# Optimization experiments

Hardware: AMD Instinct MI355X
Metric: run time of the kernel (lower is better)

## Reference

```python
import jax, jax.numpy as jnp
import numpy as np

DEPTH = 4  # truncation depth of the signature


def setup_inputs() -> dict:
    key = jax.random.key(0)
    # (N, L, C) batch of paths
    path = jax.random.normal(key, (32, 256, 8), dtype=jnp.float32)
    return {"path": path}


def _signature(path, depth):
    """Truncated path signature via Chen's relation over linear segments.

    For a linear segment with increment dx, its signature is exp(dx) in the
    tensor algebra: level j = dx^{\otimes j} / j!.  The signature of the
    concatenated path is the tensor-algebra product of segment signatures,
    computed with a scan over segments.
    """
    N, L, C = path.shape
    dx = path[:, 1:, :] - path[:, :-1, :]  # (N, L-1, C) increments

    def exp_levels(d):
        # levels of exp(d): e_j = d^{\otimes j} / j!, flattened to (N, C^j)
        levels = [d]
        for j in range(2, depth + 1):
            nxt = jnp.einsum('na,nb->nab', levels[-1], d).reshape(N, -1) / j
            levels.append(nxt)
        return levels

    def step(carry, d):
        # carry: tuple of (N, C^k) for k = 1..depth (levels of running signature)
        # Chen: new_k = sum_{i+j=k} carry_i (x) e_j, with carry_0 = e_0 = 1
        e = exp_levels(d)
        new = []
        for k in range(1, depth + 1):
            acc = carry[k - 1] + e[k - 1]  # i=k,j=0 and i=0,j=k terms
            for i in range(1, k):
                acc = acc + jnp.einsum(
                    'na,nb->nab', carry[i - 1], e[k - i - 1]
                ).reshape(N, -1)
            new.append(acc)
        return tuple(new), None

    init = tuple(jnp.zeros((N, C ** k), path.dtype) for k in range(1, depth + 1))
    final, _ = jax.lax.scan(step, init, jnp.swapaxes(dx, 0, 1))  # scan over L-1
    return jnp.concatenate(final, axis=-1)  # (N, C + C^2 + ... + C^depth)


def reference(path):
    return _signature(path, DEPTH)
```

## Files before the change

### kernel.cpp

```cpp
#include <hip/hip_runtime.h>

#define NBATCH 32
#define LPATH 256
#define NSEG 255
#define SIGLEN 4680
#define INV6 (1.0f/6.0f)
#define INV24 (1.0f/24.0f)

typedef float v2f __attribute__((ext_vector_type(2)));

struct __align__(16) CBuf {
    float T4t2[64 * 64];
    float T3b[8 * 68];
    float T2[64];
    float T1[8];
};

__device__ __forceinline__ void publish_sig(CBuf& B, const v2f S4v[32],
                                            const float S3[8], float S2, float a1a,
                                            int l, int a, int b) {
    #pragma unroll
    for (int ch = 0; ch < 32; ++ch)
        *(v2f*)&B.T4t2[ch * 128 + 2 * l] = S4v[ch];
    #pragma unroll
    for (int c = 0; c < 8; ++c)
        B.T3b[a * 68 + b * 8 + c] = S3[c];
    B.T2[l] = S2;
    if (b == 0) B.T1[a] = a1a;
}

__device__ __forceinline__ void absorb_sig(const CBuf& B, v2f S4v[32], float S3[8],
                                           float& S2, float& a1a, int l, int a, int b) {
    v2f t1v[4];
    #pragma unroll
    for (int h = 0; h < 4; ++h) t1v[h] = *(const v2f*)&B.T1[2 * h];
    const float t1a = B.T1[a];
    const float t1b = B.T1[b];
    const v2f S2v = S2, a1v = a1a;
    #pragma unroll
    for (int c = 0; c < 8; ++c) {
        const v2f S3cv = S3[c];
        #pragma unroll
        for (int h = 0; h < 4; ++h) {
            const v2f t2v = *(const v2f*)&B.T2[c * 8 + 2 * h];
            const v2f t3v = *(const v2f*)&B.T3b[b * 68 + c * 8 + 2 * h];
            const v2f t4v = *(const v2f*)&B.T4t2[(c * 4 + h) * 128 + 2 * l];
            v2f acc = S4v[c * 4 + h] + t4v;
            acc = __builtin_elementwise_fma(S3cv, t1v[h], acc);
            acc = __builtin_elementwise_fma(S2v, t2v, acc);
            acc = __builtin_elementwise_fma(a1v, t3v, acc);
            S4v[c * 4 + h] = acc;
        }
    }
    #pragma unroll
    for (int c = 0; c < 8; ++c)
        S3[c] += S2 * B.T1[c] + a1a * B.T2[b * 8 + c] + B.T3b[a * 68 + b * 8 + c];
    S2 += a1a * t1b + B.T2[l];
    a1a += t1a;
}

__global__ __launch_bounds__(512, 2) void sig_kernel(const float* __restrict__ path,
                                                     float* __restrict__ out) {
    const int n = blockIdx.x;
    const int t = threadIdx.x;
    const int w = t >> 6, l = t & 63, a = l >> 3, b = l & 7;

    __shared__ CBuf bufs[4];
    __shared__ float dbuf[2048];

    const float* prow = path + n * (LPATH * 8);
    {
        const int i4 = t * 4;
        if (i4 < NSEG * 8) {
            const float4 x0 = *(const float4*)&prow[i4];
            const float4 x1 = *(const float4*)&prow[i4 + 8];
            *(float4*)&dbuf[i4] = make_float4(x1.x - x0.x, x1.y - x0.y,
                                              x1.z - x0.z, x1.w - x0.w);
        } else {
            *(float4*)&dbuf[i4] = make_float4(0.f, 0.f, 0.f, 0.f);
        }
    }
    __syncthreads();

    v2f S4v[32];
    float S3[8];
    #pragma unroll
    for (int j = 0; j < 32; ++j) S4v[j] = (v2f)0.f;
    #pragma unroll
    for (int c = 0; c < 8; ++c) S3[c] = 0.f;
    float S2 = 0.f, a1a = 0.f;

    const float* wbase = &dbuf[w << 8];
    const float* abase = wbase + a;
    const float* bbase = wbase + b;

    #pragma unroll
    for (int ss = 0; ss < 32; ++ss) {
        const float4 dlo = *(const float4*)&wbase[ss * 8];
        const float4 dhi = *(const float4*)&wbase[ss * 8 + 4];
        const v2f dp[4] = {{dlo.x, dlo.y}, {dlo.z, dlo.w},
                           {dhi.x, dhi.y}, {dhi.z, dhi.w}};
        const float da = abase[ss * 8];
        const float db = bbase[ss * 8];
        const float dab = da * db;
        const float P = dab * INV24 + a1a * db * INV6 + S2 * 0.5f;
        const float Q = dab * INV6  + a1a * db * 0.5f + S2;
        const v2f Pv = P, Qv = Q;
        v2f Kv[4];
        #pragma unroll
        for (int h = 0; h < 4; ++h) {
            v2f S3h = {S3[2 * h], S3[2 * h + 1]};
            Kv[h] = __builtin_elementwise_fma(dp[h], Pv, S3h);
            S3h = __builtin_elementwise_fma(dp[h], Qv, S3h);
            S3[2 * h] = S3h.x; S3[2 * h + 1] = S3h.y;
        }
        #pragma unroll
        for (int c = 0; c < 8; ++c) {
            const float Kc = (c & 1) ? Kv[c >> 1].y : Kv[c >> 1].x;
            const v2f Kcv = Kc;
            #pragma unroll
            for (int h = 0; h < 4; ++h)
                S4v[c * 4 + h] = __builtin_elementwise_fma(dp[h], Kcv, S4v[c * 4 + h]);
        }
        S2 += db * (da * 0.5f + a1a);
        a1a += da;
    }

    #pragma unroll
    for (int r = 0; r < 3; ++r) {
        const int stride = 1 << r;
        const int m = (stride << 1) - 1;
        if ((w & m) == stride)
            publish_sig(bufs[w >> (r + 1)], S4v, S3, S2, a1a, l, a, b);
        __syncthreads();
        if ((w & m) == 0)
            absorb_sig(bufs[w >> (r + 1)], S4v, S3, S2, a1a, l, a, b);
        __syncthreads();
    }

    if (w == 0) {
        float* o = out + n * SIGLEN;
        if (b == 0) o[a] = a1a;
        o[8 + l] = S2;
        *(float4*)&o[72 + l * 8]     = make_float4(S3[0], S3[1], S3[2], S3[3]);
        *(float4*)&o[72 + l * 8 + 4] = make_float4(S3[4], S3[5], S3[6], S3[7]);
        #pragma unroll
        for (int ch = 0; ch < 32; ++ch)
            *(v2f*)&o[584 + l * 64 + 2 * ch] = S4v[ch];
    }
}

extern "C" void kernel_launch(void* const* d_in, const int* in_sizes, int n_in,
                              void* d_out, int out_size, void* d_ws, size_t ws_size,
                              hipStream_t stream) {
    const float* path = (const float*)d_in[0];
    float* out = (float*)d_out;
    sig_kernel<<<NBATCH, 512, 0, stream>>>(path, out);
}
```

Measured before the change: 17.95 us.

## Split each path over two blocks with half-channel waves and cross-block combine

```diff
diff --git a/kernel.cpp b/kernel.cpp
--- a/kernel.cpp
+++ b/kernel.cpp
@@ -4,149 +4,237 @@
 #define LPATH 256
 #define NSEG 255
 #define SIGLEN 4680
+#define PIMG 4712
+#define PSTRF 4720
 #define INV6 (1.0f/6.0f)
 #define INV24 (1.0f/24.0f)
 
 typedef float v2f __attribute__((ext_vector_type(2)));
+typedef unsigned long long u64;
+typedef unsigned int u32;
 
 struct __align__(16) CBuf {
-    float T4t2[64 * 64];
-    float T3b[8 * 68];
+    float T4t2[4096];
+    float T3b[544];
     float T2[64];
     float T1[8];
 };
 
-__device__ __forceinline__ void publish_sig(CBuf& B, const v2f S4v[32],
-                                            const float S3[8], float S2, float a1a,
-                                            int l, int a, int b) {
-    #pragma unroll
-    for (int ch = 0; ch < 32; ++ch)
-        *(v2f*)&B.T4t2[ch * 128 + 2 * l] = S4v[ch];
-    #pragma unroll
-    for (int c = 0; c < 8; ++c)
-        B.T3b[a * 68 + b * 8 + c] = S3[c];
-    B.T2[l] = S2;
-    if (b == 0) B.T1[a] = a1a;
-}
-
-__device__ __forceinline__ void absorb_sig(const CBuf& B, v2f S4v[32], float S3[8],
-                                           float& S2, float& a1a, int l, int a, int b) {
+__device__ __forceinline__ void publish_half(CBuf& B, const v2f S4v[16],
+                                             const float S3[4], float S2, float a1a,
+                                             int l, int a, int b, int h) {
+    #pragma unroll
+    for (int ci = 0; ci < 4; ++ci)
+        #pragma unroll
+        for (int eh = 0; eh < 4; ++eh)
+            *(v2f*)&B.T4t2[((4*h + ci)*4 + eh)*128 + 2*l] = S4v[ci*4 + eh];
+    #pragma unroll
+    for (int ci = 0; ci < 4; ++ci)
+        B.T3b[a*68 + b*8 + 4*h + ci] = S3[ci];
+    if (h == 0) {
+        B.T2[l] = S2;
+        if (b == 0) B.T1[a] = a1a;
+    }
+}
+
+__device__ __forceinline__ void absorb_half(const CBuf& B, v2f S4v[16], float S3[4],
+                                            float& S2, float& a1a,
+                                            int l, int a, int b, int h) {
     v2f t1v[4];
     #pragma unroll
-    for (int h = 0; h < 4; ++h) t1v[h] = *(const v2f*)&B.T1[2 * h];
-    const float t1a = B.T1[a];
-    const float t1b = B.T1[b];
+    for (int eh = 0; eh < 4; ++eh) t1v[eh] = *(const v2f*)&B.T1[2*eh];
+    const float t1a = B.T1[a], t1b = B.T1[b];
     const v2f S2v = S2, a1v = a1a;
     #pragma unroll
-    for (int c = 0; c < 8; ++c) {
-        const v2f S3cv = S3[c];
-        #pragma unroll
-        for (int h = 0; h < 4; ++h) {
-            const v2f t2v = *(const v2f*)&B.T2[c * 8 + 2 * h];
-            const v2f t3v = *(const v2f*)&B.T3b[b * 68 + c * 8 + 2 * h];
-            const v2f t4v = *(const v2f*)&B.T4t2[(c * 4 + h) * 128 + 2 * l];
-            v2f acc = S4v[c * 4 + h] + t4v;
-            acc = __builtin_elementwise_fma(S3cv, t1v[h], acc);
+    for (int ci = 0; ci < 4; ++ci) {
+        const int c = 4*h + ci;
+        const v2f S3cv = S3[ci];
+        #pragma unroll
+        for (int eh = 0; eh < 4; ++eh) {
+            const v2f t2v = *(const v2f*)&B.T2[c*8 + 2*eh];
+            const v2f t3v = *(const v2f*)&B.T3b[b*68 + c*8 + 2*eh];
+            const v2f t4v = *(const v2f*)&B.T4t2[(c*4 + eh)*128 + 2*l];
+            v2f acc = S4v[ci*4 + eh] + t4v;
+            acc = __builtin_elementwise_fma(S3cv, t1v[eh], acc);
             acc = __builtin_elementwise_fma(S2v, t2v, acc);
             acc = __builtin_elementwise_fma(a1v, t3v, acc);
-            S4v[c * 4 + h] = acc;
-        }
-    }
-    #pragma unroll
-    for (int c = 0; c < 8; ++c)
-        S3[c] += S2 * B.T1[c] + a1a * B.T2[b * 8 + c] + B.T3b[a * 68 + b * 8 + c];
+            S4v[ci*4 + eh] = acc;
+        }
+    }
+    #pragma unroll
+    for (int ci = 0; ci < 4; ++ci) {
+        const int c = 4*h + ci;
+        S3[ci] += S2 * B.T1[c] + a1a * B.T2[b*8 + c] + B.T3b[a*68 + b*8 + c];
+    }
     S2 += a1a * t1b + B.T2[l];
     a1a += t1a;
 }
 
-__global__ __launch_bounds__(512, 2) void sig_kernel(const float* __restrict__ path,
-                                                     float* __restrict__ out) {
-    const int n = blockIdx.x;
+__global__ __launch_bounds__(512)
+__attribute__((amdgpu_waves_per_eu(2, 2)))
+void sig_kernel(const float* __restrict__ path, float* __restrict__ pbase,
+                int* __restrict__ flags, float* __restrict__ out) {
+    const int blk = blockIdx.x;
+    const int n = blk >> 1, cb = blk & 1;
     const int t = threadIdx.x;
     const int w = t >> 6, l = t & 63, a = l >> 3, b = l & 7;
+    const int pr = w >> 1, h = w & 1;
 
     __shared__ CBuf bufs[4];
-    __shared__ float dbuf[2048];
-
-    const float* prow = path + n * (LPATH * 8);
+    __shared__ float dbuf[1024];
+    __shared__ int sh_old;
+
+    const float* prow = path + n * (LPATH*8);
     {
-        const int i4 = t * 4;
-        if (i4 < NSEG * 8) {
-            const float4 x0 = *(const float4*)&prow[i4];
-            const float4 x1 = *(const float4*)&prow[i4 + 8];
-            *(float4*)&dbuf[i4] = make_float4(x1.x - x0.x, x1.y - x0.y,
-                                              x1.z - x0.z, x1.w - x0.w);
-        } else {
-            *(float4*)&dbuf[i4] = make_float4(0.f, 0.f, 0.f, 0.f);
-        }
-    }
-    __syncthreads();
-
-    v2f S4v[32];
-    float S3[8];
-    #pragma unroll
-    for (int j = 0; j < 32; ++j) S4v[j] = (v2f)0.f;
-    #pragma unroll
-    for (int c = 0; c < 8; ++c) S3[c] = 0.f;
+        const int i2 = t * 2;
+        const int g2 = cb * 1024 + i2;
+        v2f val = {0.f, 0.f};
+        if (g2 + 1 < NSEG*8) {
+            val.x = prow[g2 + 8] - prow[g2];
+            val.y = prow[g2 + 9] - prow[g2 + 1];
+        }
+        *(v2f*)&dbuf[i2] = val;
+    }
+    __syncthreads();
+
+    v2f S4v[16];
+    float S3[4];
+    #pragma unroll
+    for (int j = 0; j < 16; ++j) S4v[j] = (v2f)0.f;
+    #pragma unroll
+    for (int ci = 0; ci < 4; ++ci) S3[ci] = 0.f;
     float S2 = 0.f, a1a = 0.f;
 
-    const float* wbase = &dbuf[w << 8];
+    const float* wbase = &dbuf[pr << 8];
     const float* abase = wbase + a;
     const float* bbase = wbase + b;
 
     #pragma unroll
     for (int ss = 0; ss < 32; ++ss) {
-        const float4 dlo = *(const float4*)&wbase[ss * 8];
-        const float4 dhi = *(const float4*)&wbase[ss * 8 + 4];
-        const v2f dp[4] = {{dlo.x, dlo.y}, {dlo.z, dlo.w},
-                           {dhi.x, dhi.y}, {dhi.z, dhi.w}};
-        const float da = abase[ss * 8];
-        const float db = bbase[ss * 8];
+        const float4 dlo = *(const float4*)&wbase[ss*8];
+        const float4 dhi = *(const float4*)&wbase[ss*8 + 4];
+        const v2f dp0 = {dlo.x, dlo.y}, dp1 = {dlo.z, dlo.w};
+        const v2f dp2 = {dhi.x, dhi.y}, dp3 = {dhi.z, dhi.w};
+        const v2f dcl = h ? dp2 : dp0;
+        const v2f dch = h ? dp3 : dp1;
+        const float da = abase[ss*8];
+        const float db = bbase[ss*8];
         const float dab = da * db;
-        const float P = dab * INV24 + a1a * db * INV6 + S2 * 0.5f;
-        const float Q = dab * INV6  + a1a * db * 0.5f + S2;
+        const float P = dab*INV24 + a1a*db*INV6 + S2*0.5f;
+        const float Q = dab*INV6  + a1a*db*0.5f + S2;
         const v2f Pv = P, Qv = Q;
-        v2f Kv[4];
-        #pragma unroll
-        for (int h = 0; h < 4; ++h) {
-            v2f S3h = {S3[2 * h], S3[2 * h + 1]};
-            Kv[h] = __builtin_elementwise_fma(dp[h], Pv, S3h);
-            S3h = __builtin_elementwise_fma(dp[h], Qv, S3h);
-            S3[2 * h] = S3h.x; S3[2 * h + 1] = S3h.y;
-        }
-        #pragma unroll
-        for (int c = 0; c < 8; ++c) {
-            const float Kc = (c & 1) ? Kv[c >> 1].y : Kv[c >> 1].x;
-            const v2f Kcv = Kc;
-            #pragma unroll
-            for (int h = 0; h < 4; ++h)
-                S4v[c * 4 + h] = __builtin_elementwise_fma(dp[h], Kcv, S4v[c * 4 + h]);
-        }
-        S2 += db * (da * 0.5f + a1a);
+        v2f K0, K1;
+        {
+            v2f s3l = {S3[0], S3[1]};
+            K0 = __builtin_elementwise_fma(dcl, Pv, s3l);
+            s3l = __builtin_elementwise_fma(dcl, Qv, s3l);
+            S3[0] = s3l.x; S3[1] = s3l.y;
+        }
+        {
+            v2f s3h = {S3[2], S3[3]};
+            K1 = __builtin_elementwise_fma(dch, Pv, s3h);
+            s3h = __builtin_elementwise_fma(dch, Qv, s3h);
+            S3[2] = s3h.x; S3[3] = s3h.y;
+        }
+        const float Kc[4] = {K0.x, K0.y, K1.x, K1.y};
+        #pragma unroll
+        for (int ci = 0; ci < 4; ++ci) {
+            const v2f Kcv = Kc[ci];
+            S4v[ci*4+0] = __builtin_elementwise_fma(dp0, Kcv, S4v[ci*4+0]);
+            S4v[ci*4+1] = __builtin_elementwise_fma(dp1, Kcv, S4v[ci*4+1]);
+            S4v[ci*4+2] = __builtin_elementwise_fma(dp2, Kcv, S4v[ci*4+2]);
+            S4v[ci*4+3] = __builtin_elementwise_fma(dp3, Kcv, S4v[ci*4+3]);
+        }
+        S2 += db * (da*0.5f + a1a);
         a1a += da;
     }
 
-    #pragma unroll
-    for (int r = 0; r < 3; ++r) {
-        const int stride = 1 << r;
-        const int m = (stride << 1) - 1;
-        if ((w & m) == stride)
-            publish_sig(bufs[w >> (r + 1)], S4v, S3, S2, a1a, l, a, b);
+    if (pr & 1) publish_half(bufs[pr >> 1], S4v, S3, S2, a1a, l, a, b, h);
+    __syncthreads();
+    if (!(pr & 1)) absorb_half(bufs[pr >> 1], S4v, S3, S2, a1a, l, a, b, h);
+    __syncthreads();
+    if (pr == 2) publish_half(bufs[0], S4v, S3, S2, a1a, l, a, b, h);
+    __syncthreads();
+    if (pr == 0) absorb_half(bufs[0], S4v, S3, S2, a1a, l, a, b, h);
+    __syncthreads();
+
+    if (pr == 0) {
+        float* p = pbase + (size_t)blk * PSTRF;
+        #pragma unroll
+        for (int ci = 0; ci < 4; ++ci)
+            #pragma unroll
+            for (int eh = 0; eh < 4; ++eh) {
+                u64 uv; __builtin_memcpy(&uv, &S4v[ci*4 + eh], 8);
+                __hip_atomic_store((u64*)&p[((4*h + ci)*4 + eh)*128 + 2*l], uv,
+                                   __ATOMIC_RELAXED, __HIP_MEMORY_SCOPE_AGENT);
+            }
+        #pragma unroll
+        for (int ci = 0; ci < 4; ++ci) {
+            u32 uv; __builtin_memcpy(&uv, &S3[ci], 4);
+            __hip_atomic_store((u32*)&p[4096 + a*68 + b*8 + 4*h + ci], uv,
+                               __ATOMIC_RELAXED, __HIP_MEMORY_SCOPE_AGENT);
+        }
+        if (h == 0) {
+            u32 uv; __builtin_memcpy(&uv, &S2, 4);
+            __hip_atomic_store((u32*)&p[4640 + l], uv,
+                               __ATOMIC_RELAXED, __HIP_MEMORY_SCOPE_AGENT);
+            if (b == 0) {
+                u32 u1; __builtin_memcpy(&u1, &a1a, 4);
+                __hip_atomic_store((u32*)&p[4704 + a], u1,
+                                   __ATOMIC_RELAXED, __HIP_MEMORY_SCOPE_AGENT);
+            }
+        }
+        asm volatile("s_waitcnt vmcnt(0)" ::: "memory");
+    }
+    __syncthreads();
+    if (t == 0)
+        sh_old = __hip_atomic_fetch_add(&flags[n], 1, __ATOMIC_RELAXED,
+                                        __HIP_MEMORY_SCOPE_AGENT);
+    __syncthreads();
+    if (sh_old != 1) return;
+
+    {
+        const u64* src = (const u64*)(pbase + (size_t)(n*2 + (cb ^ 1)) * PSTRF);
+        u64* dst = (u64*)&bufs[2];
+        for (int i = t; i < PIMG/2; i += 512)
+            dst[i] = __hip_atomic_load(&src[i], __ATOMIC_RELAXED,
+                                       __HIP_MEMORY_SCOPE_AGENT);
+    }
+    __syncthreads();
+
+    if (cb == 1) {
+        if (pr == 0) publish_half(bufs[3], S4v, S3, S2, a1a, l, a, b, h);
         __syncthreads();
-        if ((w & m) == 0)
-            absorb_sig(bufs[w >> (r + 1)], S4v, S3, S2, a1a, l, a, b);
-        __syncthreads();
-    }
-
-    if (w == 0) {
+        if (pr == 0) {
+            #pragma unroll
+            for (int ci = 0; ci < 4; ++ci)
+                #pragma unroll
+                for (int eh = 0; eh < 4; ++eh)
+                    S4v[ci*4 + eh] =
+                        *(const v2f*)&bufs[2].T4t2[((4*h + ci)*4 + eh)*128 + 2*l];
+            #pragma unroll
+            for (int ci = 0; ci < 4; ++ci)
+                S3[ci] = bufs[2].T3b[a*68 + b*8 + 4*h + ci];
+            S2 = bufs[2].T2[l];
+            a1a = bufs[2].T1[a];
+            absorb_half(bufs[3], S4v, S3, S2, a1a, l, a, b, h);
+        }
+    } else {
+        if (pr == 0) absorb_half(bufs[2], S4v, S3, S2, a1a, l, a, b, h);
+    }
+
+    if (pr == 0) {
         float* o = out + n * SIGLEN;
-        if (b == 0) o[a] = a1a;
-        o[8 + l] = S2;
-        *(float4*)&o[72 + l * 8]     = make_float4(S3[0], S3[1], S3[2], S3[3]);
-        *(float4*)&o[72 + l * 8 + 4] = make_float4(S3[4], S3[5], S3[6], S3[7]);
-        #pragma unroll
-        for (int ch = 0; ch < 32; ++ch)
-            *(v2f*)&o[584 + l * 64 + 2 * ch] = S4v[ch];
+        if (h == 0) {
+            if (b == 0) o[a] = a1a;
+            o[8 + l] = S2;
+        }
+        *(float4*)&o[72 + l*8 + 4*h] = make_float4(S3[0], S3[1], S3[2], S3[3]);
+        #pragma unroll
+        for (int ci = 0; ci < 4; ++ci)
+            #pragma unroll
+            for (int eh = 0; eh < 4; ++eh)
+                *(v2f*)&o[584 + l*64 + (4*h + ci)*8 + 2*eh] = S4v[ci*4 + eh];
     }
 }
 
@@ -155,5 +243,8 @@
                               hipStream_t stream) {
     const float* path = (const float*)d_in[0];
     float* out = (float*)d_out;
-    sig_kernel<<<NBATCH, 512, 0, stream>>>(path, out);
-}
+    int* flags = (int*)d_ws;
+    float* pbase = (float*)d_ws + 256;
+    hipMemsetAsync(d_ws, 0, NBATCH * sizeof(int), stream);
+    sig_kernel<<<NBATCH * 2, 512, 0, stream>>>(path, pbase, flags, out);
+}
```

After: 21.42 us. 19.3% more time.
